# Kernel tuning notes

Hardware: AMD Instinct MI355X
Metric: run time of the kernel (lower is better)

Reference implementation:

```python
import jax, jax.numpy as jnp
import numpy as np

# Module hyperparameters (from init_kwargs)
MEAN = (0.485, 0.456, 0.406)
STD = (0.229, 0.224, 0.225)
P_ERASE = 0.5
SCALE = (0.02, 0.33)
RATIO = (0.3, 3.3)


def setup_inputs() -> dict:
    key = jax.random.key(0)
    x = jax.random.uniform(key, (64, 3, 384, 384), dtype=jnp.float32)
    mean = jnp.array(MEAN, dtype=jnp.float32).reshape(1, 3, 1, 1)
    std = jnp.array(STD, dtype=jnp.float32).reshape(1, 3, 1, 1)
    return {"x": x, "mean": mean, "std": std}


def reference(x, mean, std):
    """Normalize then apply batched random erasing (training mode).

    Faithful to the torch module, but the per-sample Python loop is replaced
    by a single vectorized mask computation over the whole batch.
    """
    B, C, H, W = x.shape
    xn = (x - mean) / std

    k = jax.random.key(42)
    kp, ka, kr, kt, kl, kn = jax.random.split(k, 6)

    # Per-sample: keep-or-erase coin flip, target area, aspect ratio.
    apply = jax.random.uniform(kp, (B,)) <= P_ERASE
    area = float(H * W)
    ta = jax.random.uniform(ka, (B,), minval=SCALE[0], maxval=SCALE[1]) * area
    ar = jax.random.uniform(kr, (B,), minval=RATIO[0], maxval=RATIO[1])
    h_e = jnp.round(jnp.sqrt(ta * ar)).astype(jnp.int32)
    w_e = jnp.round(jnp.sqrt(ta / ar)).astype(jnp.int32)
    valid = apply & (h_e < H) & (w_e < W)

    # Uniform integer top/left in [0, H-h_e] / [0, W-w_e] (matches randint high=H-h_e+1).
    top = jnp.floor(jax.random.uniform(kt, (B,)) * (H - h_e + 1).astype(jnp.float32)).astype(jnp.int32)
    left = jnp.floor(jax.random.uniform(kl, (B,)) * (W - w_e + 1).astype(jnp.float32)).astype(jnp.int32)

    rows = jnp.arange(H)[None, :]                       # (1, H)
    cols = jnp.arange(W)[None, :]                       # (1, W)
    rmask = (rows >= top[:, None]) & (rows < (top + h_e)[:, None])    # (B, H)
    cmask = (cols >= left[:, None]) & (cols < (left + w_e)[:, None])  # (B, W)
    mask = valid[:, None, None] & rmask[:, :, None] & cmask[:, None, :]  # (B, H, W)

    noise = jax.random.normal(kn, x.shape, dtype=x.dtype)
    return jnp.where(mask[:, None, :, :], noise, xn)
```

## Files before the change

kernel.cpp:

```cpp
#include <hip/hip_runtime.h>
#include <cstring>
#include <cstdint>
#include <cmath>

#define B_IMG 64
#define C_IMG 3
#define H_IMG 384
#define W_IMG 384
#define PLANE (H_IMG * W_IMG)
#define N_TOT (B_IMG * C_IMG * PLANE)
#define N4    (N_TOT / 4)
#define V4_PER_BLOCK 512
#define BLOCKS (N4 / V4_PER_BLOCK)

typedef float nfloat4 __attribute__((ext_vector_type(4)));

struct Rect { int t, b, l, r; };
struct Params { Rect rc[B_IMG]; };

__host__ __device__ inline uint32_t rotl32(uint32_t x, uint32_t r) {
  return (x << r) | (x >> (32u - r));
}

__host__ __device__ inline void tf2x32(uint32_t k0, uint32_t k1,
                                       uint32_t x0, uint32_t x1,
                                       uint32_t& o0, uint32_t& o1) {
  const uint32_t ks2 = k0 ^ k1 ^ 0x1BD11BDAu;
  x0 += k0; x1 += k1;
  x0 += x1; x1 = rotl32(x1, 13); x1 ^= x0;
  x0 += x1; x1 = rotl32(x1, 15); x1 ^= x0;
  x0 += x1; x1 = rotl32(x1, 26); x1 ^= x0;
  x0 += x1; x1 = rotl32(x1,  6); x1 ^= x0;
  x0 += k1; x1 += ks2 + 1u;
  x0 += x1; x1 = rotl32(x1, 17); x1 ^= x0;
  x0 += x1; x1 = rotl32(x1, 29); x1 ^= x0;
  x0 += x1; x1 = rotl32(x1, 16); x1 ^= x0;
  x0 += x1; x1 = rotl32(x1, 24); x1 ^= x0;
  x0 += ks2; x1 += k0 + 2u;
  x0 += x1; x1 = rotl32(x1, 13); x1 ^= x0;
  x0 += x1; x1 = rotl32(x1, 15); x1 ^= x0;
  x0 += x1; x1 = rotl32(x1, 26); x1 ^= x0;
  x0 += x1; x1 = rotl32(x1,  6); x1 ^= x0;
  x0 += k0; x1 += k1 + 3u;
  x0 += x1; x1 = rotl32(x1, 17); x1 ^= x0;
  x0 += x1; x1 = rotl32(x1, 29); x1 ^= x0;
  x0 += x1; x1 = rotl32(x1, 16); x1 ^= x0;
  x0 += x1; x1 = rotl32(x1, 24); x1 ^= x0;
  x0 += k1; x1 += ks2 + 4u;
  x0 += x1; x1 = rotl32(x1, 13); x1 ^= x0;
  x0 += x1; x1 = rotl32(x1, 15); x1 ^= x0;
  x0 += x1; x1 = rotl32(x1, 26); x1 ^= x0;
  x0 += x1; x1 = rotl32(x1,  6); x1 ^= x0;
  x0 += ks2; x1 += k0 + 5u;
  o0 = x0; o1 = x1;
}

__host__ __device__ inline float unit_from_bits(uint32_t bits) {
  uint32_t fb = (bits >> 9) | 0x3f800000u;
  float f;
#ifdef __HIP_DEVICE_COMPILE__
  f = __uint_as_float(fb);
#else
  memcpy(&f, &fb, 4);
#endif
  return f - 1.0f;
}

__host__ __device__ inline uint32_t rb_partitionable(uint32_t k0, uint32_t k1, uint32_t idx) {
  uint32_t o0, o1;
  tf2x32(k0, k1, 0u, idx, o0, o1);
  return o0 ^ o1;
}

__device__ inline float noise_val(uint32_t idx, uint32_t kn0, uint32_t kn1) {
  const float LO = -0x1.fffffep-1f;
  uint32_t bits = rb_partitionable(kn0, kn1, idx);
  float f = unit_from_bits(bits);
  float u = __fadd_rn(__fmul_rn(f, 2.0f), LO);
  u = fmaxf(LO, u);
  float t  = __fmul_rn(u, u);
  float wv = -log1pf(-t);
  float p;
  if (wv < 5.0f) {
    float ww = __fadd_rn(wv, -2.5f);
    p = 2.81022636e-08f;
    p = __fadd_rn(__fmul_rn(p, ww),  3.43273939e-07f);
    p = __fadd_rn(__fmul_rn(p, ww), -3.5233877e-06f);
    p = __fadd_rn(__fmul_rn(p, ww), -4.39150654e-06f);
    p = __fadd_rn(__fmul_rn(p, ww),  0.00021858087f);
    p = __fadd_rn(__fmul_rn(p, ww), -0.00125372503f);
    p = __fadd_rn(__fmul_rn(p, ww), -0.00417768164f);
    p = __fadd_rn(__fmul_rn(p, ww),  0.246640727f);
    p = __fadd_rn(__fmul_rn(p, ww),  1.50140941f);
  } else {
    float ww = __fadd_rn(__fsqrt_rn(wv), -3.0f);
    p = -0.000200214257f;
    p = __fadd_rn(__fmul_rn(p, ww),  0.000100950558f);
    p = __fadd_rn(__fmul_rn(p, ww),  0.00134934322f);
    p = __fadd_rn(__fmul_rn(p, ww), -0.00367342844f);
    p = __fadd_rn(__fmul_rn(p, ww),  0.00573950773f);
    p = __fadd_rn(__fmul_rn(p, ww), -0.0076224613f);
    p = __fadd_rn(__fmul_rn(p, ww),  0.00943887047f);
    p = __fadd_rn(__fmul_rn(p, ww),  1.00167406f);
    p = __fadd_rn(__fmul_rn(p, ww),  2.83297682f);
  }
  float r = __fmul_rn(p, u);
  return __fmul_rn(1.41421356237f, r);
}

static void compute_host_params(Params& P, uint32_t& kn0, uint32_t& kn1) {
#pragma clang fp contract(off)
  uint32_t keys[6][2];
  for (uint32_t i = 0; i < 6; i++)
    tf2x32(0u, 42u, 0u, i, keys[i][0], keys[i][1]);
  kn0 = keys[5][0]; kn1 = keys[5][1];

  for (int b = 0; b < B_IMG; b++) {
    float u[5];
    for (int k = 0; k < 5; k++)
      u[k] = unit_from_bits(rb_partitionable(keys[k][0], keys[k][1], (uint32_t)b));

    float up = u[0];
    float da = 0.33f - 0.02f;
    float ua = u[1] * da;  ua = ua + 0.02f;  ua = fmaxf(0.02f, ua);
    float ta = ua * 147456.0f;
    float dr = 3.3f - 0.3f;
    float ur = u[2] * dr;  ur = ur + 0.3f;   ur = fmaxf(0.3f, ur);

    int he = (int)rintf(sqrtf(ta * ur));
    int we = (int)rintf(sqrtf(ta / ur));
    bool valid = (up <= 0.5f) && (he < H_IMG) && (we < W_IMG);

    int top  = (int)floorf(u[3] * (float)(H_IMG - he + 1));
    int left = (int)floorf(u[4] * (float)(W_IMG - we + 1));

    if (valid) { P.rc[b].t = top;  P.rc[b].b = top + he; P.rc[b].l = left; P.rc[b].r = left + we; }
    else       { P.rc[b].t = 0;    P.rc[b].b = 0;        P.rc[b].l = 0;    P.rc[b].r = 0; }
  }
}

__global__ __launch_bounds__(256) void erase_norm_kernel(
    const float* __restrict__ x, const float* __restrict__ mean,
    const float* __restrict__ stdv, float* __restrict__ out,
    Params P, uint32_t kn0, uint32_t kn1) {
  const int t = threadIdx.x;
  const int plane = blockIdx.x / (PLANE / (V4_PER_BLOCK * 4));
  const int c = plane % C_IMG;
  const int b = plane / C_IMG;

  const nfloat4* __restrict__ x4 = reinterpret_cast<const nfloat4*>(x);
  nfloat4* __restrict__ o4 = reinterpret_cast<nfloat4*>(out);

  const int i0 = blockIdx.x * V4_PER_BLOCK + t;
  const int i1 = i0 + 256;
  const nfloat4 v0 = __builtin_nontemporal_load(&x4[i0]);
  const nfloat4 v1 = __builtin_nontemporal_load(&x4[i1]);

  const float m  = mean[c];
  const float rs = 1.0f / stdv[c];
  const float nm = -m * rs;
  const Rect rc = P.rc[b];
  const int planeBase = plane * PLANE;

  nfloat4 vv[2] = {v0, v1};
  int idx4[2] = {i0, i1};
#pragma unroll
  for (int j = 0; j < 2; j++) {
    nfloat4 o;
    o.x = fmaf(vv[j].x, rs, nm);
    o.y = fmaf(vv[j].y, rs, nm);
    o.z = fmaf(vv[j].z, rs, nm);
    o.w = fmaf(vv[j].w, rs, nm);

    const int base = idx4[j] * 4;
    const int rel  = base - planeBase;
    const int h = rel / W_IMG;
    const int w = rel - h * W_IMG;
    if (h >= rc.t && h < rc.b && w < rc.r && (w + 3) >= rc.l) {
      if (w     >= rc.l && w     < rc.r) o.x = noise_val((uint32_t)(base + 0), kn0, kn1);
      if (w + 1 >= rc.l && w + 1 < rc.r) o.y = noise_val((uint32_t)(base + 1), kn0, kn1);
      if (w + 2 >= rc.l && w + 2 < rc.r) o.z = noise_val((uint32_t)(base + 2), kn0, kn1);
      if (w + 3 >= rc.l && w + 3 < rc.r) o.w = noise_val((uint32_t)(base + 3), kn0, kn1);
    }
    o4[idx4[j]] = o;
  }
}

extern "C" void kernel_launch(void* const* d_in, const int* in_sizes, int n_in,
                              void* d_out, int out_size, void* d_ws, size_t ws_size,
                              hipStream_t stream) {
  const float* x    = (const float*)d_in[0];
  const float* mean = (const float*)d_in[1];
  const float* stdv = (const float*)d_in[2];
  float* out = (float*)d_out;

  Params P;
  uint32_t kn0, kn1;
  compute_host_params(P, kn0, kn1);

  erase_norm_kernel<<<BLOCKS, 256, 0, stream>>>(x, mean, stdv, out, P, kn0, kn1);
}
```

Measured before the change: 198.9 us.

## Split normalize and erase into separate kernels, writing noise only inside rectangles

Normalization now runs as a pure streaming kernel with no per-element rectangle checks. A second kernel launched on the same stream overwrites only the erased rectangle of each plane with Threefry-based normal noise, and returns early for planes with no erase. This removes divergent noise computation from the bandwidth-bound pass. In exchange the erased region is written twice, which adds a second launch and extra scattered writes to it.

```diff
diff --git a/kernel.cpp b/kernel.cpp
--- a/kernel.cpp
+++ b/kernel.cpp
@@ -139,14 +139,12 @@
   }
 }
 
-__global__ __launch_bounds__(256) void erase_norm_kernel(
+__global__ __launch_bounds__(256) void norm_kernel(
     const float* __restrict__ x, const float* __restrict__ mean,
-    const float* __restrict__ stdv, float* __restrict__ out,
-    Params P, uint32_t kn0, uint32_t kn1) {
+    const float* __restrict__ stdv, float* __restrict__ out) {
   const int t = threadIdx.x;
   const int plane = blockIdx.x / (PLANE / (V4_PER_BLOCK * 4));
   const int c = plane % C_IMG;
-  const int b = plane / C_IMG;
 
   const nfloat4* __restrict__ x4 = reinterpret_cast<const nfloat4*>(x);
   nfloat4* __restrict__ o4 = reinterpret_cast<nfloat4*>(out);
@@ -159,30 +157,36 @@
   const float m  = mean[c];
   const float rs = 1.0f / stdv[c];
   const float nm = -m * rs;
+
+  nfloat4 o0, o1;
+  o0.x = fmaf(v0.x, rs, nm);
+  o0.y = fmaf(v0.y, rs, nm);
+  o0.z = fmaf(v0.z, rs, nm);
+  o0.w = fmaf(v0.w, rs, nm);
+  o1.x = fmaf(v1.x, rs, nm);
+  o1.y = fmaf(v1.y, rs, nm);
+  o1.z = fmaf(v1.z, rs, nm);
+  o1.w = fmaf(v1.w, rs, nm);
+  o4[i0] = o0;
+  o4[i1] = o1;
+}
+
+#define ROWCHUNKS 16
+
+__global__ __launch_bounds__(256) void erase_patch_kernel(
+    float* __restrict__ out, Params P, uint32_t kn0, uint32_t kn1) {
+  const int bc = blockIdx.x;
+  const int b = bc / C_IMG;
   const Rect rc = P.rc[b];
-  const int planeBase = plane * PLANE;
-
-  nfloat4 vv[2] = {v0, v1};
-  int idx4[2] = {i0, i1};
-#pragma unroll
-  for (int j = 0; j < 2; j++) {
-    nfloat4 o;
-    o.x = fmaf(vv[j].x, rs, nm);
-    o.y = fmaf(vv[j].y, rs, nm);
-    o.z = fmaf(vv[j].z, rs, nm);
-    o.w = fmaf(vv[j].w, rs, nm);
-
-    const int base = idx4[j] * 4;
-    const int rel  = base - planeBase;
-    const int h = rel / W_IMG;
-    const int w = rel - h * W_IMG;
-    if (h >= rc.t && h < rc.b && w < rc.r && (w + 3) >= rc.l) {
-      if (w     >= rc.l && w     < rc.r) o.x = noise_val((uint32_t)(base + 0), kn0, kn1);
-      if (w + 1 >= rc.l && w + 1 < rc.r) o.y = noise_val((uint32_t)(base + 1), kn0, kn1);
-      if (w + 2 >= rc.l && w + 2 < rc.r) o.z = noise_val((uint32_t)(base + 2), kn0, kn1);
-      if (w + 3 >= rc.l && w + 3 < rc.r) o.w = noise_val((uint32_t)(base + 3), kn0, kn1);
+  if (rc.t == rc.b) return;
+
+  const int planeBase = bc * PLANE;
+  for (int h = rc.t + blockIdx.y; h < rc.b; h += ROWCHUNKS) {
+    const int rowBase = planeBase + h * W_IMG;
+    for (int w = rc.l + threadIdx.x; w < rc.r; w += 256) {
+      const int idx = rowBase + w;
+      out[idx] = noise_val((uint32_t)idx, kn0, kn1);
     }
-    o4[idx4[j]] = o;
   }
 }
 
@@ -198,5 +202,6 @@
   uint32_t kn0, kn1;
   compute_host_params(P, kn0, kn1);
 
-  erase_norm_kernel<<<BLOCKS, 256, 0, stream>>>(x, mean, stdv, out, P, kn0, kn1);
-}
+  norm_kernel<<<BLOCKS, 256, 0, stream>>>(x, mean, stdv, out);
+  erase_patch_kernel<<<dim3(B_IMG * C_IMG, ROWCHUNKS), 256, 0, stream>>>(out, P, kn0, kn1);
+}
```

After: 235.7 us. 18.5% more time.
